# Optimization experiments

Measured on AMD Instinct MI355X. Metric: run time of the kernel, lower is better.

Reference implementation:

```python
import jax, jax.numpy as jnp
import numpy as np

B, T, D, F, H, HID, OUT = 256, 512, 768, 1024, 8, 512, 256
EPS = 1e-5

def setup_inputs() -> dict:
    key = jax.random.key(0)
    ks = jax.random.split(key, 16)
    s = lambda fan_in: 1.0 / np.sqrt(fan_in)
    return {
        "x": jax.random.normal(ks[0], (B, F), jnp.float32),
        "text_feat": jax.random.normal(ks[1], (B, T, D), jnp.float32),
        "attention_mask": jax.random.randint(ks[2], (B, T), 0, 2, jnp.int32),
        # cross-attention params (torch Linear weight layout [out,in])
        "Wq": jax.random.normal(ks[3], (F, F), jnp.float32) * s(F),
        "bq": jnp.zeros((F,), jnp.float32),
        "Wk": jax.random.normal(ks[4], (F, D), jnp.float32) * s(D),
        "bk": jnp.zeros((F,), jnp.float32),
        "Wv": jax.random.normal(ks[5], (F, D), jnp.float32) * s(D),
        "bv": jnp.zeros((F,), jnp.float32),
        "Wo": jax.random.normal(ks[6], (F, F), jnp.float32) * s(F),
        "bo": jnp.zeros((F,), jnp.float32),
        # MLP: hidden Linear -> BatchNorm1d -> GELU, then output Linear
        "W1": jax.random.normal(ks[7], (HID, F), jnp.float32) * s(F),
        "b1": jnp.zeros((HID,), jnp.float32),
        "gamma": jnp.ones((HID,), jnp.float32),
        "beta": jnp.zeros((HID,), jnp.float32),
        "W2": jax.random.normal(ks[8], (OUT, HID), jnp.float32) * s(HID),
        "b2": jnp.zeros((OUT,), jnp.float32),
    }

def _forward(x, text_feat, attention_mask, Wq, bq, Wk, bk, Wv, bv, Wo, bo,
             W1, b1, gamma, beta, W2, b2):
    d = F // H
    q = (x @ Wq.T + bq).reshape(B, H, d)                      # [B,H,d] (q_len=1)
    k = (text_feat @ Wk.T + bk).reshape(B, T, H, d)           # [B,T,H,d]
    v = (text_feat @ Wv.T + bv).reshape(B, T, H, d)
    attn = jnp.einsum('bhd,bthd->bht', q, k) / jnp.sqrt(jnp.float32(d))
    attn = jnp.where(attention_mask[:, None, :] == 0, -jnp.inf, attn)
    attn = jax.nn.softmax(attn, axis=-1)                       # [B,H,T]
    out = jnp.einsum('bht,bthd->bhd', attn, v).reshape(B, F)
    out = out @ Wo.T + bo
    # MLP hidden: linear -> BatchNorm1d (training batch stats) -> GELU (exact)
    h = out @ W1.T + b1
    mu = jnp.mean(h, axis=0)
    var = jnp.var(h, axis=0)
    h = (h - mu) / jnp.sqrt(var + EPS) * gamma + beta
    h = jax.nn.gelu(h, approximate=False)
    return h @ W2.T + b2

def reference(x, text_feat, attention_mask, Wq, bq, Wk, bk, Wv, bv, Wo, bo,
              W1, b1, gamma, beta, W2, b2):
    return _forward(x, text_feat, attention_mask, Wq, bq, Wk, bk, Wv, bv, Wo, bo,
                    W1, b1, gamma, beta, W2, b2)
```

## Files before the change

kernel.cpp:

```cpp
#include <hip/hip_runtime.h>
#include <math.h>

#define Bb   256
#define Tt   512
#define Dd   768
#define Ff   1024
#define Hh   8
#define HIDh 512
#define OUTo 256

__device__ __forceinline__ void tr_tile(const float* __restrict__ in,
                                        float* __restrict__ out,
                                        int R, int C, int cx, int ry,
                                        float (*tile)[33])
{
    int c0 = cx * 32, r0 = ry * 32;
    int tx = threadIdx.x & 31, ty = threadIdx.x >> 5;
#pragma unroll
    for (int i = 0; i < 32; i += 8)
        tile[ty + i][tx] = in[(size_t)(r0 + ty + i) * C + c0 + tx];
    __syncthreads();
#pragma unroll
    for (int i = 0; i < 32; i += 8)
        out[(size_t)(c0 + ty + i) * R + r0 + tx] = tile[tx][ty + i];
}

__global__ __launch_bounds__(256) void prep(const float* __restrict__ Wq, float* __restrict__ WqT,
                                            const float* __restrict__ Wo, float* __restrict__ WoT,
                                            const float* __restrict__ Wv, float* __restrict__ WvT,
                                            const float* __restrict__ W1, float* __restrict__ W1T,
                                            const float* __restrict__ W2, float* __restrict__ W2T,
                                            const float* __restrict__ Wk, float* __restrict__ WkT)
{
    __shared__ float tile[32][33];
    int idx = blockIdx.x;
    if (idx < 1024) {
        tr_tile(Wq, WqT, 1024, 1024, idx & 31, idx >> 5, tile);
    } else if (idx < 2048) {
        int i2 = idx - 1024;
        tr_tile(Wo, WoT, 1024, 1024, i2 & 31, i2 >> 5, tile);
    } else if (idx < 2816) {
        int i2 = idx - 2048;
        tr_tile(Wv, WvT, 1024, 768, i2 % 24, i2 / 24, tile);
    } else if (idx < 3328) {
        int i2 = idx - 2816;
        tr_tile(W1, W1T, 512, 1024, i2 & 31, i2 >> 5, tile);
    } else if (idx < 3456) {
        int i2 = idx - 3328;
        tr_tile(W2, W2T, 256, 512, i2 & 15, i2 >> 4, tile);
    } else {
        int i2 = idx - 3456;
        int i = i2 >> 3, h = i2 & 7;
        for (int j = threadIdx.x; j < 768; j += 256)
            WkT[(size_t)(i * 8 + h) * 768 + j] = Wk[(size_t)(h * 128 + i) * 768 + j];
    }
}

#define FMA16(acc, a, w0, w1, w2, w3)                         \
    acc.x = fmaf(a.x, w0.x, acc.x); acc.y = fmaf(a.x, w0.y, acc.y); \
    acc.z = fmaf(a.x, w0.z, acc.z); acc.w = fmaf(a.x, w0.w, acc.w); \
    acc.x = fmaf(a.y, w1.x, acc.x); acc.y = fmaf(a.y, w1.y, acc.y); \
    acc.z = fmaf(a.y, w1.z, acc.z); acc.w = fmaf(a.y, w1.w, acc.w); \
    acc.x = fmaf(a.z, w2.x, acc.x); acc.y = fmaf(a.z, w2.y, acc.y); \
    acc.z = fmaf(a.z, w2.z, acc.z); acc.w = fmaf(a.z, w2.w, acc.w); \
    acc.x = fmaf(a.w, w3.x, acc.x); acc.y = fmaf(a.w, w3.y, acc.y); \
    acc.z = fmaf(a.w, w3.z, acc.z); acc.w = fmaf(a.w, w3.w, acc.w);

template<int CT, int RT, int R, int KS>
__global__ __launch_bounds__(256, 4) void gemm_sk(const float* __restrict__ A, int strideA,
                                                  const float* __restrict__ Wt, int N,
                                                  float* __restrict__ Cslab, int M)
{
    constexpr int CG = CT / 4;
    constexpr int RG = RT / R;
    static_assert(CG * RG == 256, "bad tile");
    const int cg = threadIdx.x % CG;
    const int rg = threadIdx.x / CG;
    const int cb = blockIdx.x, rb = blockIdx.y, ks = blockIdx.z;
    const int n0 = cb * CT + cg * 4;
    const int r0 = rb * RT;
    const int k0 = ks * KS;

    __shared__ float As[RT][KS + 4];
    for (int e = threadIdx.x * 4; e < RT * KS; e += 1024) {
        int r = e / KS, k = e % KS;
        *(float4*)&As[r][k] = *(const float4*)&A[(size_t)(r0 + r) * strideA + k0 + k];
    }
    __syncthreads();

    float4 acc[R];
#pragma unroll
    for (int rr = 0; rr < R; ++rr) acc[rr] = make_float4(0.f, 0.f, 0.f, 0.f);
    const float* wp = Wt + (size_t)k0 * N + n0;
#pragma unroll 2
    for (int k = 0; k < KS; k += 4) {
        float4 w0 = *(const float4*)&wp[(size_t)(k + 0) * N];
        float4 w1 = *(const float4*)&wp[(size_t)(k + 1) * N];
        float4 w2 = *(const float4*)&wp[(size_t)(k + 2) * N];
        float4 w3 = *(const float4*)&wp[(size_t)(k + 3) * N];
#pragma unroll
        for (int rr = 0; rr < R; ++rr) {
            float4 a = *(const float4*)&As[rg * R + rr][k];
            FMA16(acc[rr], a, w0, w1, w2, w3)
        }
    }
    float* cp = Cslab + (size_t)ks * M * N;
#pragma unroll
    for (int rr = 0; rr < R; ++rr)
        *(float4*)&cp[(size_t)(r0 + rg * R + rr) * N + n0] = acc[rr];
}

template<int CT, int RT, int R, int KS, int S>
__global__ __launch_bounds__(256, 4) void gemm_skf(const float* __restrict__ slabs,
                                                   size_t slabstride, int strideA,
                                                   const float* __restrict__ bias,
                                                   const float* __restrict__ Wt, int N,
                                                   float* __restrict__ Cslab, int M)
{
    constexpr int CG = CT / 4;
    constexpr int RG = RT / R;
    static_assert(CG * RG == 256, "bad tile");
    const int cg = threadIdx.x % CG;
    const int rg = threadIdx.x / CG;
    const int cb = blockIdx.x, rb = blockIdx.y, ks = blockIdx.z;
    const int n0 = cb * CT + cg * 4;
    const int r0 = rb * RT;
    const int k0 = ks * KS;

    __shared__ float As[RT][KS + 4];
    for (int e = threadIdx.x * 4; e < RT * KS; e += 1024) {
        int r = e / KS, k = e % KS;
        float4 acc = *(const float4*)&bias[k0 + k];
#pragma unroll
        for (int s = 0; s < S; ++s) {
            float4 v = *(const float4*)&slabs[(size_t)s * slabstride + (size_t)(r0 + r) * strideA + k0 + k];
            acc.x += v.x; acc.y += v.y; acc.z += v.z; acc.w += v.w;
        }
        *(float4*)&As[r][k] = acc;
    }
    __syncthreads();

    float4 acc[R];
#pragma unroll
    for (int rr = 0; rr < R; ++rr) acc[rr] = make_float4(0.f, 0.f, 0.f, 0.f);
    const float* wp = Wt + (size_t)k0 * N + n0;
#pragma unroll 2
    for (int k = 0; k < KS; k += 4) {
        float4 w0 = *(const float4*)&wp[(size_t)(k + 0) * N];
        float4 w1 = *(const float4*)&wp[(size_t)(k + 1) * N];
        float4 w2 = *(const float4*)&wp[(size_t)(k + 2) * N];
        float4 w3 = *(const float4*)&wp[(size_t)(k + 3) * N];
#pragma unroll
        for (int rr = 0; rr < R; ++rr) {
            float4 a = *(const float4*)&As[rg * R + rr][k];
            FMA16(acc[rr], a, w0, w1, w2, w3)
        }
    }
    float* cp = Cslab + (size_t)ks * M * N;
#pragma unroll
    for (int rr = 0; rr < R; ++rr)
        *(float4*)&cp[(size_t)(r0 + rg * R + rr) * N + n0] = acc[rr];
}

__global__ __launch_bounds__(256, 4) void qk_gemm(const float* __restrict__ qslab,
                                                  const float* __restrict__ bq,
                                                  const float* __restrict__ WkT,
                                                  float* __restrict__ qkfull)
{
    const int cg = threadIdx.x & 15;
    const int rg = threadIdx.x >> 4;
    const int cb = blockIdx.x, rb = blockIdx.y;
    const int n0 = cb * 64 + cg * 4;
    const int r0 = rb * 16;
    const int aoff = ((cb * 64) / 768) * 128;

    __shared__ float As[16][132];
    for (int e = threadIdx.x * 4; e < 16 * 128; e += 1024) {
        int r = e >> 7, k = e & 127;
        float4 acc = *(const float4*)&bq[aoff + k];
#pragma unroll
        for (int s = 0; s < 8; ++s) {
            float4 v = *(const float4*)&qslab[(size_t)s * 262144 + (size_t)(r0 + r) * 1024 + aoff + k];
            acc.x += v.x; acc.y += v.y; acc.z += v.z; acc.w += v.w;
        }
        *(float4*)&As[r][k] = acc;
    }
    __syncthreads();

    float4 acc = make_float4(0.f, 0.f, 0.f, 0.f);
    const float* wp = WkT + n0;
#pragma unroll 4
    for (int k = 0; k < 128; k += 4) {
        float4 w0 = *(const float4*)&wp[(size_t)(k + 0) * 6144];
        float4 w1 = *(const float4*)&wp[(size_t)(k + 1) * 6144];
        float4 w2 = *(const float4*)&wp[(size_t)(k + 2) * 6144];
        float4 w3 = *(const float4*)&wp[(size_t)(k + 3) * 6144];
        float4 a = *(const float4*)&As[rg][k];
        FMA16(acc, a, w0, w1, w2, w3)
    }
    *(float4*)&qkfull[(size_t)(r0 + rg) * 6144 + n0] = acc;
}

__global__ __launch_bounds__(256, 2) void attn_part(const float* __restrict__ text,
                                                    const int* __restrict__ mask,
                                                    const float* __restrict__ qk,
                                                    float* __restrict__ pctx,
                                                    float* __restrict__ psum)
{
    const int bx   = blockIdx.x;
    const int b    = bx >> 2;
    const int qt   = bx & 3;
    const int tid  = threadIdx.x;
    const int wv   = tid >> 6;
    const int lane = tid & 63;

    __shared__ float qk_s[Hh][Dd];
    __shared__ float ctx_s[Hh][Dd];
    __shared__ float wsum_s[4][Hh];
    __shared__ int   list_s[128];
    __shared__ int   wcnt_s[2];

    const float* qkp = qk + (size_t)b * (Hh * Dd);
    float* qf = (float*)qk_s;
    float* cf = (float*)ctx_s;
    for (int e = tid * 4; e < Hh * Dd; e += 1024) {
        *(float4*)&qf[e] = *(const float4*)&qkp[e];
        *(float4*)&cf[e] = make_float4(0.f, 0.f, 0.f, 0.f);
    }

    int m = 0, pre = 0, t = 0;
    if (wv < 2) {
        t = qt * 128 + wv * 64 + lane;
        m = mask[(size_t)b * Tt + t];
        unsigned long long bal = __ballot(m != 0);
        pre = __popcll(bal & ((1ull << lane) - 1ull));
        if (lane == 0) wcnt_s[wv] = __popcll(bal);
    }
    __syncthreads();
    if (wv < 2 && m) {
        int base = wv ? wcnt_s[0] : 0;
        list_s[base + pre] = t;
    }
    __syncthreads();
    const int cnt = wcnt_s[0] + wcnt_s[1];

    float s[Hh] = {0.f, 0.f, 0.f, 0.f, 0.f, 0.f, 0.f, 0.f};
    float4 cr[Hh][3];
#pragma unroll
    for (int h = 0; h < Hh; ++h)
#pragma unroll
        for (int c = 0; c < 3; ++c) cr[h][c] = make_float4(0.f, 0.f, 0.f, 0.f);

    const float scale = 0.08838834764831845f;
    const float* tbase = text + (size_t)b * Tt * Dd;

    int e = wv;
    float4 xa0, xa1, xa2;
    if (e < cnt) {
        const float* tp = tbase + (size_t)list_s[e] * Dd + 4 * lane;
        xa0 = *(const float4*)(tp);
        xa1 = *(const float4*)(tp + 256);
        xa2 = *(const float4*)(tp + 512);
    }
    while (e < cnt) {
        int en = e + 4;
        float4 xb0 = xa0, xb1 = xa1, xb2 = xa2;
        if (en < cnt) {
            const float* tp = tbase + (size_t)list_s[en] * Dd + 4 * lane;
            xb0 = *(const float4*)(tp);
            xb1 = *(const float4*)(tp + 256);
            xb2 = *(const float4*)(tp + 512);
        }
        float p[Hh];
#pragma unroll
        for (int h = 0; h < Hh; ++h) {
            const float* qh = &qk_s[h][4 * lane];
            float4 a0 = *(const float4*)(qh);
            float4 a1 = *(const float4*)(qh + 256);
            float4 a2 = *(const float4*)(qh + 512);
            float acc;
            acc = a0.x * xa0.x;
            acc = fmaf(a0.y, xa0.y, acc);
            acc = fmaf(a0.z, xa0.z, acc);
            acc = fmaf(a0.w, xa0.w, acc);
            acc = fmaf(a1.x, xa1.x, acc);
            acc = fmaf(a1.y, xa1.y, acc);
            acc = fmaf(a1.z, xa1.z, acc);
            acc = fmaf(a1.w, xa1.w, acc);
            acc = fmaf(a2.x, xa2.x, acc);
            acc = fmaf(a2.y, xa2.y, acc);
            acc = fmaf(a2.z, xa2.z, acc);
            acc = fmaf(a2.w, xa2.w, acc);
            p[h] = acc;
        }
#pragma unroll
        for (int h = 0; h < Hh; ++h) {
            float v = p[h];
            v += __shfl_xor(v, 1);
            v += __shfl_xor(v, 2);
            v += __shfl_xor(v, 4);
            v += __shfl_xor(v, 8);
            v += __shfl_xor(v, 16);
            v += __shfl_xor(v, 32);
            float w = __expf(v * scale);
            s[h] += w;
            cr[h][0].x = fmaf(w, xa0.x, cr[h][0].x);
            cr[h][0].y = fmaf(w, xa0.y, cr[h][0].y);
            cr[h][0].z = fmaf(w, xa0.z, cr[h][0].z);
            cr[h][0].w = fmaf(w, xa0.w, cr[h][0].w);
            cr[h][1].x = fmaf(w, xa1.x, cr[h][1].x);
            cr[h][1].y = fmaf(w, xa1.y, cr[h][1].y);
            cr[h][1].z = fmaf(w, xa1.z, cr[h][1].z);
            cr[h][1].w = fmaf(w, xa1.w, cr[h][1].w);
            cr[h][2].x = fmaf(w, xa2.x, cr[h][2].x);
            cr[h][2].y = fmaf(w, xa2.y, cr[h][2].y);
            cr[h][2].z = fmaf(w, xa2.z, cr[h][2].z);
            cr[h][2].w = fmaf(w, xa2.w, cr[h][2].w);
        }
        xa0 = xb0; xa1 = xb1; xa2 = xb2;
        e = en;
    }

    if (lane == 0) {
#pragma unroll
        for (int h = 0; h < Hh; ++h) wsum_s[wv][h] = s[h];
    }

    for (int w4 = 0; w4 < 4; ++w4) {
        __syncthreads();
        if (wv == w4) {
#pragma unroll
            for (int h = 0; h < Hh; ++h) {
                float* cp = &ctx_s[h][4 * lane];
#pragma unroll
                for (int c = 0; c < 3; ++c) {
                    float4 cur = *(float4*)(cp + c * 256);
                    cur.x += cr[h][c].x;
                    cur.y += cr[h][c].y;
                    cur.z += cr[h][c].z;
                    cur.w += cr[h][c].w;
                    *(float4*)(cp + c * 256) = cur;
                }
            }
        }
    }
    __syncthreads();

    if (tid < Hh) {
        float S = wsum_s[0][tid] + wsum_s[1][tid] + wsum_s[2][tid] + wsum_s[3][tid];
        psum[(size_t)bx * Hh + tid] = S;
    }
    float* outp = pctx + (size_t)bx * (Hh * Dd);
    for (int e2 = tid * 4; e2 < Hh * Dd; e2 += 1024)
        *(float4*)&outp[e2] = *(const float4*)&cf[e2];
}

__global__ __launch_bounds__(256, 4) void v_gemm(const float* __restrict__ pctx,
                                                 const float* __restrict__ psum,
                                                 const float* __restrict__ WvT,
                                                 float* __restrict__ aoslab)
{
    const int cg = threadIdx.x & 31;
    const int rg = threadIdx.x >> 5;
    const int h = blockIdx.x, rb = blockIdx.y, ks = blockIdx.z;
    const int n0 = h * 128 + cg * 4;
    const int r0 = rb * 32;
    const int k0 = ks * 128;

    __shared__ float As[32][132];
    __shared__ float sv[32];

    if (threadIdx.x < 32) {
        int row = r0 + threadIdx.x;
        float S = 0.f;
#pragma unroll
        for (int i = 0; i < 4; ++i) S += psum[(size_t)(row * 4 + i) * Hh + h];
        sv[threadIdx.x] = 1.0f / S;
    }
    __syncthreads();
    for (int e = threadIdx.x * 4; e < 32 * 128; e += 1024) {
        int r = e >> 7, k = e & 127;
        size_t col = (size_t)h * 768 + k0 + k;
        float4 acc = make_float4(0.f, 0.f, 0.f, 0.f);
#pragma unroll
        for (int i = 0; i < 4; ++i) {
            float4 v = *(const float4*)&pctx[((size_t)(r0 + r) * 4 + i) * 6144 + col];
            acc.x += v.x; acc.y += v.y; acc.z += v.z; acc.w += v.w;
        }
        float svv = sv[r];
        acc.x *= svv; acc.y *= svv; acc.z *= svv; acc.w *= svv;
        *(float4*)&As[r][k] = acc;
    }
    __syncthreads();

    float4 acc[4];
#pragma unroll
    for (int rr = 0; rr < 4; ++rr) acc[rr] = make_float4(0.f, 0.f, 0.f, 0.f);
    const float* wp = WvT + (size_t)k0 * 1024 + n0;
#pragma unroll 2
    for (int k = 0; k < 128; k += 4) {
        float4 w0 = *(const float4*)&wp[(size_t)(k + 0) * 1024];
        float4 w1 = *(const float4*)&wp[(size_t)(k + 1) * 1024];
        float4 w2 = *(const float4*)&wp[(size_t)(k + 2) * 1024];
        float4 w3 = *(const float4*)&wp[(size_t)(k + 3) * 1024];
#pragma unroll
        for (int rr = 0; rr < 4; ++rr) {
            float4 a = *(const float4*)&As[rg * 4 + rr][k];
            FMA16(acc[rr], a, w0, w1, w2, w3)
        }
    }
    float* cp = aoslab + (size_t)ks * 262144;
#pragma unroll
    for (int rr = 0; rr < 4; ++rr)
        *(float4*)&cp[(size_t)(r0 + rg * 4 + rr) * 1024 + n0] = acc[rr];
}

__global__ __launch_bounds__(256) void bn_stats2(const float* __restrict__ h1slab,
                                                 const float* __restrict__ b1,
                                                 const float* __restrict__ gamma,
                                                 const float* __restrict__ beta,
                                                 float* __restrict__ scl,
                                                 float* __restrict__ shf)
{
    int c8 = threadIdx.x & 7, rg = threadIdx.x >> 3;
    int c = blockIdx.x * 8 + c8;
    float bias = b1[c];
    float sum = 0.f, sq = 0.f;
    for (int r = rg; r < Bb; r += 32) {
        float v = bias;
#pragma unroll
        for (int s = 0; s < 8; ++s)
            v += h1slab[(size_t)s * 131072 + (size_t)r * HIDh + c];
        sum += v;
        sq = fmaf(v, v, sq);
    }
    __shared__ float ss[32][8], sq_[32][8];
    ss[rg][c8] = sum; sq_[rg][c8] = sq;
    for (int off = 16; off > 0; off >>= 1) {
        __syncthreads();
        if (rg < off) { ss[rg][c8] += ss[rg + off][c8]; sq_[rg][c8] += sq_[rg + off][c8]; }
    }
    __syncthreads();
    if (rg == 0) {
        float mu  = ss[0][c8] * (1.0f / Bb);
        float var = sq_[0][c8] * (1.0f / Bb) - mu * mu;
        float g   = gamma[c] * rsqrtf(var + 1e-5f);
        scl[c] = g;
        shf[c] = fmaf(-mu, g, beta[c]);
    }
}

__global__ __launch_bounds__(256, 4) void gelu2(const float* __restrict__ h1slab,
                                                const float* __restrict__ b1,
                                                const float* __restrict__ scl,
                                                const float* __restrict__ shf,
                                                const float* __restrict__ W2T,
                                                const float* __restrict__ b2,
                                                float* __restrict__ out)
{
    const int cg = threadIdx.x & 15;
    const int rg = threadIdx.x >> 4;
    const int n0 = blockIdx.x * 64 + cg * 4;
    const int r0 = blockIdx.y * 16;

    __shared__ float As[16][132];
    float4 acc = make_float4(0.f, 0.f, 0.f, 0.f);

    for (int k0 = 0; k0 < HIDh; k0 += 128) {
        __syncthreads();
        for (int e = threadIdx.x * 4; e < 2048; e += 1024) {
            int r = e >> 7, k = e & 127;
            float4 v = *(const float4*)&b1[k0 + k];
#pragma unroll
            for (int s = 0; s < 8; ++s) {
                float4 u = *(const float4*)&h1slab[(size_t)s * 131072 + (size_t)(r0 + r) * HIDh + k0 + k];
                v.x += u.x; v.y += u.y; v.z += u.z; v.w += u.w;
            }
            float4 sc = *(const float4*)&scl[k0 + k];
            float4 sh = *(const float4*)&shf[k0 + k];
            float4 z;
            z.x = fmaf(v.x, sc.x, sh.x);
            z.y = fmaf(v.y, sc.y, sh.y);
            z.z = fmaf(v.z, sc.z, sh.z);
            z.w = fmaf(v.w, sc.w, sh.w);
            z.x = 0.5f * z.x * (1.0f + erff(z.x * 0.70710678118654752f));
            z.y = 0.5f * z.y * (1.0f + erff(z.y * 0.70710678118654752f));
            z.z = 0.5f * z.z * (1.0f + erff(z.z * 0.70710678118654752f));
            z.w = 0.5f * z.w * (1.0f + erff(z.w * 0.70710678118654752f));
            *(float4*)&As[r][k] = z;
        }
        __syncthreads();
        const float* wp = W2T + (size_t)k0 * OUTo + n0;
#pragma unroll 2
        for (int k = 0; k < 128; k += 4) {
            float4 w0 = *(const float4*)&wp[(size_t)(k + 0) * OUTo];
            float4 w1 = *(const float4*)&wp[(size_t)(k + 1) * OUTo];
            float4 w2 = *(const float4*)&wp[(size_t)(k + 2) * OUTo];
            float4 w3 = *(const float4*)&wp[(size_t)(k + 3) * OUTo];
            float4 a = *(const float4*)&As[rg][k];
            FMA16(acc, a, w0, w1, w2, w3)
        }
    }

    float4 bvv = *(const float4*)&b2[n0];
    acc.x += bvv.x; acc.y += bvv.y; acc.z += bvv.z; acc.w += bvv.w;
    *(float4*)&out[(size_t)(r0 + rg) * OUTo + n0] = acc;
}

extern "C" void kernel_launch(void* const* d_in, const int* in_sizes, int n_in,
                              void* d_out, int out_size, void* d_ws, size_t ws_size,
                              hipStream_t stream)
{
    const float* x     = (const float*)d_in[0];
    const float* text  = (const float*)d_in[1];
    const int*   amask = (const int*)d_in[2];
    const float* Wq    = (const float*)d_in[3];
    const float* bq    = (const float*)d_in[4];
    const float* Wk    = (const float*)d_in[5];
    const float* Wv    = (const float*)d_in[7];
    const float* bv    = (const float*)d_in[8];
    const float* Wo    = (const float*)d_in[9];
    const float* bo    = (const float*)d_in[10];
    const float* W1    = (const float*)d_in[11];
    const float* b1    = (const float*)d_in[12];
    const float* gamma = (const float*)d_in[13];
    const float* beta  = (const float*)d_in[14];
    const float* W2    = (const float*)d_in[15];
    const float* b2    = (const float*)d_in[16];

    float* ws     = (float*)d_ws;
    float* WqT    = ws;
    float* WoT    = WqT    + 1048576;
    float* WkT    = WoT    + 1048576;
    float* WvT    = WkT    + 786432;
    float* W1T    = WvT    + 786432;
    float* W2T    = W1T    + 524288;
    float* qslab  = W2T    + 131072;
    float* qkfull = qslab  + 2097152;
    float* pctx   = qkfull + 1572864;
    float* psum   = pctx   + 6291456;
    float* aoslab = psum   + 8192;
    float* oslab  = aoslab + 1572864;
    float* h1slab = oslab  + 2097152;
    float* scl    = h1slab + 1048576;
    float* shf    = scl    + 512;

    prep<<<4480, 256, 0, stream>>>(Wq, WqT, Wo, WoT, Wv, WvT, W1, W1T, W2, W2T, Wk, WkT);

    gemm_sk<128, 32, 4, 128><<<dim3(8, 8, 8), 256, 0, stream>>>(x, 1024, WqT, 1024, qslab, 256);

    qk_gemm<<<dim3(96, 16), 256, 0, stream>>>(qslab, bq, WkT, qkfull);

    attn_part<<<1024, 256, 0, stream>>>(text, amask, qkfull, pctx, psum);

    v_gemm<<<dim3(8, 8, 6), 256, 0, stream>>>(pctx, psum, WvT, aoslab);

    gemm_skf<128, 32, 4, 128, 6><<<dim3(8, 8, 8), 256, 0, stream>>>(aoslab, 262144, 1024, bv, WoT, 1024, oslab, 256);

    gemm_skf<64, 32, 2, 128, 8><<<dim3(8, 8, 8), 256, 0, stream>>>(oslab, 262144, 1024, bo, W1T, 512, h1slab, 256);

    bn_stats2<<<64, 256, 0, stream>>>(h1slab, b1, gamma, beta, scl, shf);

    gelu2<<<dim3(4, 16), 256, 0, stream>>>(h1slab, b1, scl, shf, W2T, b2, (float*)d_out);
}
```

Before: 251.9 us.

## Split split-K reductions into separate kernels, rework attention and GEMM tiles

Split-K partial sums are now reduced by dedicated reduce_add kernels instead of being summed redundantly inside every consumer block. GEMM tiles shrink and grids grow for more parallelism, and unroll factors go up. The attention kernel now uses 512-thread blocks over half the sequence and processes two tokens per iteration. Weight transposes and the Wk copy use float4 accesses. The cost is extra kernel launches and extra workspace round trips through global memory.

```diff
diff --git a/kernel.cpp b/kernel.cpp
--- a/kernel.cpp
+++ b/kernel.cpp
@@ -9,20 +9,26 @@
 #define HIDh 512
 #define OUTo 256
 
-__device__ __forceinline__ void tr_tile(const float* __restrict__ in,
-                                        float* __restrict__ out,
-                                        int R, int C, int cx, int ry,
-                                        float (*tile)[33])
+__device__ __forceinline__ void tr_tile4(const float* __restrict__ in,
+                                         float* __restrict__ out,
+                                         int R, int C, int cx, int ry,
+                                         float (*tile)[33])
 {
     int c0 = cx * 32, r0 = ry * 32;
-    int tx = threadIdx.x & 31, ty = threadIdx.x >> 5;
-#pragma unroll
-    for (int i = 0; i < 32; i += 8)
-        tile[ty + i][tx] = in[(size_t)(r0 + ty + i) * C + c0 + tx];
-    __syncthreads();
-#pragma unroll
-    for (int i = 0; i < 32; i += 8)
-        out[(size_t)(c0 + ty + i) * R + r0 + tx] = tile[tx][ty + i];
+    int r  = threadIdx.x >> 3;
+    int c4 = (threadIdx.x & 7) * 4;
+    float4 v = *(const float4*)&in[(size_t)(r0 + r) * C + c0 + c4];
+    tile[r][c4 + 0] = v.x;
+    tile[r][c4 + 1] = v.y;
+    tile[r][c4 + 2] = v.z;
+    tile[r][c4 + 3] = v.w;
+    __syncthreads();
+    float4 o;
+    o.x = tile[c4 + 0][r];
+    o.y = tile[c4 + 1][r];
+    o.z = tile[c4 + 2][r];
+    o.w = tile[c4 + 3][r];
+    *(float4*)&out[(size_t)(c0 + r) * R + r0 + c4] = o;
 }
 
 __global__ __launch_bounds__(256) void prep(const float* __restrict__ Wq, float* __restrict__ WqT,
@@ -35,24 +41,27 @@
     __shared__ float tile[32][33];
     int idx = blockIdx.x;
     if (idx < 1024) {
-        tr_tile(Wq, WqT, 1024, 1024, idx & 31, idx >> 5, tile);
+        tr_tile4(Wq, WqT, 1024, 1024, idx & 31, idx >> 5, tile);
     } else if (idx < 2048) {
         int i2 = idx - 1024;
-        tr_tile(Wo, WoT, 1024, 1024, i2 & 31, i2 >> 5, tile);
+        tr_tile4(Wo, WoT, 1024, 1024, i2 & 31, i2 >> 5, tile);
     } else if (idx < 2816) {
         int i2 = idx - 2048;
-        tr_tile(Wv, WvT, 1024, 768, i2 % 24, i2 / 24, tile);
+        tr_tile4(Wv, WvT, 1024, 768, i2 % 24, i2 / 24, tile);
     } else if (idx < 3328) {
         int i2 = idx - 2816;
-        tr_tile(W1, W1T, 512, 1024, i2 & 31, i2 >> 5, tile);
+        tr_tile4(W1, W1T, 512, 1024, i2 & 31, i2 >> 5, tile);
     } else if (idx < 3456) {
         int i2 = idx - 3328;
-        tr_tile(W2, W2T, 256, 512, i2 & 15, i2 >> 4, tile);
+        tr_tile4(W2, W2T, 256, 512, i2 & 15, i2 >> 4, tile);
     } else {
         int i2 = idx - 3456;
         int i = i2 >> 3, h = i2 & 7;
-        for (int j = threadIdx.x; j < 768; j += 256)
-            WkT[(size_t)(i * 8 + h) * 768 + j] = Wk[(size_t)(h * 128 + i) * 768 + j];
+        if (threadIdx.x < 192) {
+            int j = threadIdx.x * 4;
+            *(float4*)&WkT[(size_t)(i * 8 + h) * 768 + j] =
+                *(const float4*)&Wk[(size_t)(h * 128 + i) * 768 + j];
+        }
     }
 }
 
@@ -76,10 +85,9 @@
     static_assert(CG * RG == 256, "bad tile");
     const int cg = threadIdx.x % CG;
     const int rg = threadIdx.x / CG;
-    const int cb = blockIdx.x, rb = blockIdx.y, ks = blockIdx.z;
-    const int n0 = cb * CT + cg * 4;
-    const int r0 = rb * RT;
-    const int k0 = ks * KS;
+    const int n0 = blockIdx.x * CT + cg * 4;
+    const int r0 = blockIdx.y * RT;
+    const int k0 = blockIdx.z * KS;
 
     __shared__ float As[RT][KS + 4];
     for (int e = threadIdx.x * 4; e < RT * KS; e += 1024) {
@@ -92,7 +100,7 @@
 #pragma unroll
     for (int rr = 0; rr < R; ++rr) acc[rr] = make_float4(0.f, 0.f, 0.f, 0.f);
     const float* wp = Wt + (size_t)k0 * N + n0;
-#pragma unroll 2
+#pragma unroll 4
     for (int k = 0; k < KS; k += 4) {
         float4 w0 = *(const float4*)&wp[(size_t)(k + 0) * N];
         float4 w1 = *(const float4*)&wp[(size_t)(k + 1) * N];
@@ -104,66 +112,30 @@
             FMA16(acc[rr], a, w0, w1, w2, w3)
         }
     }
-    float* cp = Cslab + (size_t)ks * M * N;
+    float* cp = Cslab + (size_t)blockIdx.z * M * N;
 #pragma unroll
     for (int rr = 0; rr < R; ++rr)
         *(float4*)&cp[(size_t)(r0 + rg * R + rr) * N + n0] = acc[rr];
 }
 
-template<int CT, int RT, int R, int KS, int S>
-__global__ __launch_bounds__(256, 4) void gemm_skf(const float* __restrict__ slabs,
-                                                   size_t slabstride, int strideA,
-                                                   const float* __restrict__ bias,
-                                                   const float* __restrict__ Wt, int N,
-                                                   float* __restrict__ Cslab, int M)
-{
-    constexpr int CG = CT / 4;
-    constexpr int RG = RT / R;
-    static_assert(CG * RG == 256, "bad tile");
-    const int cg = threadIdx.x % CG;
-    const int rg = threadIdx.x / CG;
-    const int cb = blockIdx.x, rb = blockIdx.y, ks = blockIdx.z;
-    const int n0 = cb * CT + cg * 4;
-    const int r0 = rb * RT;
-    const int k0 = ks * KS;
-
-    __shared__ float As[RT][KS + 4];
-    for (int e = threadIdx.x * 4; e < RT * KS; e += 1024) {
-        int r = e / KS, k = e % KS;
-        float4 acc = *(const float4*)&bias[k0 + k];
-#pragma unroll
-        for (int s = 0; s < S; ++s) {
-            float4 v = *(const float4*)&slabs[(size_t)s * slabstride + (size_t)(r0 + r) * strideA + k0 + k];
-            acc.x += v.x; acc.y += v.y; acc.z += v.z; acc.w += v.w;
-        }
-        *(float4*)&As[r][k] = acc;
-    }
-    __syncthreads();
-
-    float4 acc[R];
-#pragma unroll
-    for (int rr = 0; rr < R; ++rr) acc[rr] = make_float4(0.f, 0.f, 0.f, 0.f);
-    const float* wp = Wt + (size_t)k0 * N + n0;
-#pragma unroll 2
-    for (int k = 0; k < KS; k += 4) {
-        float4 w0 = *(const float4*)&wp[(size_t)(k + 0) * N];
-        float4 w1 = *(const float4*)&wp[(size_t)(k + 1) * N];
-        float4 w2 = *(const float4*)&wp[(size_t)(k + 2) * N];
-        float4 w3 = *(const float4*)&wp[(size_t)(k + 3) * N];
-#pragma unroll
-        for (int rr = 0; rr < R; ++rr) {
-            float4 a = *(const float4*)&As[rg * R + rr][k];
-            FMA16(acc[rr], a, w0, w1, w2, w3)
-        }
-    }
-    float* cp = Cslab + (size_t)ks * M * N;
-#pragma unroll
-    for (int rr = 0; rr < R; ++rr)
-        *(float4*)&cp[(size_t)(r0 + rg * R + rr) * N + n0] = acc[rr];
-}
-
-__global__ __launch_bounds__(256, 4) void qk_gemm(const float* __restrict__ qslab,
-                                                  const float* __restrict__ bq,
+template<int S>
+__global__ __launch_bounds__(256) void reduce_add(const float* __restrict__ slabs,
+                                                  size_t slabstride,
+                                                  const float* __restrict__ bias,
+                                                  float* __restrict__ out, int N, int total)
+{
+    int i4 = (blockIdx.x * 256 + threadIdx.x) * 4;
+    if (i4 >= total) return;
+    float4 acc = *(const float4*)&bias[i4 % N];
+#pragma unroll
+    for (int s = 0; s < S; ++s) {
+        float4 v = *(const float4*)(slabs + (size_t)s * slabstride + i4);
+        acc.x += v.x; acc.y += v.y; acc.z += v.z; acc.w += v.w;
+    }
+    *(float4*)&out[i4] = acc;
+}
+
+__global__ __launch_bounds__(256, 4) void qk_gemm(const float* __restrict__ qfull,
                                                   const float* __restrict__ WkT,
                                                   float* __restrict__ qkfull)
 {
@@ -175,15 +147,9 @@
     const int aoff = ((cb * 64) / 768) * 128;
 
     __shared__ float As[16][132];
-    for (int e = threadIdx.x * 4; e < 16 * 128; e += 1024) {
+    for (int e = threadIdx.x * 4; e < 2048; e += 1024) {
         int r = e >> 7, k = e & 127;
-        float4 acc = *(const float4*)&bq[aoff + k];
-#pragma unroll
-        for (int s = 0; s < 8; ++s) {
-            float4 v = *(const float4*)&qslab[(size_t)s * 262144 + (size_t)(r0 + r) * 1024 + aoff + k];
-            acc.x += v.x; acc.y += v.y; acc.z += v.z; acc.w += v.w;
-        }
-        *(float4*)&As[r][k] = acc;
+        *(float4*)&As[r][k] = *(const float4*)&qfull[(size_t)(r0 + r) * 1024 + aoff + k];
     }
     __syncthreads();
 
@@ -201,48 +167,68 @@
     *(float4*)&qkfull[(size_t)(r0 + rg) * 6144 + n0] = acc;
 }
 
-__global__ __launch_bounds__(256, 2) void attn_part(const float* __restrict__ text,
+__device__ __forceinline__ float dot12(float4 a0, float4 a1, float4 a2,
+                                       float4 x0, float4 x1, float4 x2)
+{
+    float acc;
+    acc = a0.x * x0.x;
+    acc = fmaf(a0.y, x0.y, acc);
+    acc = fmaf(a0.z, x0.z, acc);
+    acc = fmaf(a0.w, x0.w, acc);
+    acc = fmaf(a1.x, x1.x, acc);
+    acc = fmaf(a1.y, x1.y, acc);
+    acc = fmaf(a1.z, x1.z, acc);
+    acc = fmaf(a1.w, x1.w, acc);
+    acc = fmaf(a2.x, x2.x, acc);
+    acc = fmaf(a2.y, x2.y, acc);
+    acc = fmaf(a2.z, x2.z, acc);
+    acc = fmaf(a2.w, x2.w, acc);
+    return acc;
+}
+
+__global__ __launch_bounds__(512, 1) void attn_part(const float* __restrict__ text,
                                                     const int* __restrict__ mask,
                                                     const float* __restrict__ qk,
                                                     float* __restrict__ pctx,
                                                     float* __restrict__ psum)
 {
     const int bx   = blockIdx.x;
-    const int b    = bx >> 2;
-    const int qt   = bx & 3;
+    const int b    = bx >> 1;
+    const int hf   = bx & 1;
     const int tid  = threadIdx.x;
     const int wv   = tid >> 6;
     const int lane = tid & 63;
 
     __shared__ float qk_s[Hh][Dd];
     __shared__ float ctx_s[Hh][Dd];
-    __shared__ float wsum_s[4][Hh];
-    __shared__ int   list_s[128];
-    __shared__ int   wcnt_s[2];
+    __shared__ float wsum_s[8][Hh];
+    __shared__ int   list_s[256];
+    __shared__ int   wcnt_s[4];
 
     const float* qkp = qk + (size_t)b * (Hh * Dd);
     float* qf = (float*)qk_s;
     float* cf = (float*)ctx_s;
-    for (int e = tid * 4; e < Hh * Dd; e += 1024) {
+    for (int e = tid * 4; e < Hh * Dd; e += 2048) {
         *(float4*)&qf[e] = *(const float4*)&qkp[e];
         *(float4*)&cf[e] = make_float4(0.f, 0.f, 0.f, 0.f);
     }
 
     int m = 0, pre = 0, t = 0;
-    if (wv < 2) {
-        t = qt * 128 + wv * 64 + lane;
+    if (wv < 4) {
+        t = hf * 256 + wv * 64 + lane;
         m = mask[(size_t)b * Tt + t];
         unsigned long long bal = __ballot(m != 0);
         pre = __popcll(bal & ((1ull << lane) - 1ull));
         if (lane == 0) wcnt_s[wv] = __popcll(bal);
     }
     __syncthreads();
-    if (wv < 2 && m) {
-        int base = wv ? wcnt_s[0] : 0;
+    if (wv < 4 && m) {
+        int base = 0;
+        for (int w = 0; w < wv; ++w) base += wcnt_s[w];
         list_s[base + pre] = t;
     }
     __syncthreads();
-    const int cnt = wcnt_s[0] + wcnt_s[1];
+    const int cnt = wcnt_s[0] + wcnt_s[1] + wcnt_s[2] + wcnt_s[3];
 
     float s[Hh] = {0.f, 0.f, 0.f, 0.f, 0.f, 0.f, 0.f, 0.f};
     float4 cr[Hh][3];
@@ -254,70 +240,96 @@
     const float scale = 0.08838834764831845f;
     const float* tbase = text + (size_t)b * Tt * Dd;
 
-    int e = wv;
-    float4 xa0, xa1, xa2;
+    int e = wv * 2;
+    bool vy = false;
+    float4 xa0, xa1, xa2, ya0, ya1, ya2;
     if (e < cnt) {
         const float* tp = tbase + (size_t)list_s[e] * Dd + 4 * lane;
         xa0 = *(const float4*)(tp);
         xa1 = *(const float4*)(tp + 256);
         xa2 = *(const float4*)(tp + 512);
+        vy = (e + 1 < cnt);
+        const float* tq = tbase + (size_t)list_s[vy ? e + 1 : e] * Dd + 4 * lane;
+        ya0 = *(const float4*)(tq);
+        ya1 = *(const float4*)(tq + 256);
+        ya2 = *(const float4*)(tq + 512);
     }
     while (e < cnt) {
-        int en = e + 4;
-        float4 xb0 = xa0, xb1 = xa1, xb2 = xa2;
-        if (en < cnt) {
+        int en = e + 16;
+        bool nv  = en < cnt;
+        bool nvy = (en + 1 < cnt);
+        float4 xb0 = xa0, xb1 = xa1, xb2 = xa2, yb0 = ya0, yb1 = ya1, yb2 = ya2;
+        if (nv) {
             const float* tp = tbase + (size_t)list_s[en] * Dd + 4 * lane;
             xb0 = *(const float4*)(tp);
             xb1 = *(const float4*)(tp + 256);
             xb2 = *(const float4*)(tp + 512);
-        }
-        float p[Hh];
+            const float* tq = tbase + (size_t)list_s[nvy ? en + 1 : en] * Dd + 4 * lane;
+            yb0 = *(const float4*)(tq);
+            yb1 = *(const float4*)(tq + 256);
+            yb2 = *(const float4*)(tq + 512);
+        }
+
+        float px[Hh], py[Hh];
 #pragma unroll
         for (int h = 0; h < Hh; ++h) {
             const float* qh = &qk_s[h][4 * lane];
             float4 a0 = *(const float4*)(qh);
             float4 a1 = *(const float4*)(qh + 256);
             float4 a2 = *(const float4*)(qh + 512);
-            float acc;
-            acc = a0.x * xa0.x;
-            acc = fmaf(a0.y, xa0.y, acc);
-            acc = fmaf(a0.z, xa0.z, acc);
-            acc = fmaf(a0.w, xa0.w, acc);
-            acc = fmaf(a1.x, xa1.x, acc);
-            acc = fmaf(a1.y, xa1.y, acc);
-            acc = fmaf(a1.z, xa1.z, acc);
-            acc = fmaf(a1.w, xa1.w, acc);
-            acc = fmaf(a2.x, xa2.x, acc);
-            acc = fmaf(a2.y, xa2.y, acc);
-            acc = fmaf(a2.z, xa2.z, acc);
-            acc = fmaf(a2.w, xa2.w, acc);
-            p[h] = acc;
+            px[h] = dot12(a0, a1, a2, xa0, xa1, xa2);
+            py[h] = dot12(a0, a1, a2, ya0, ya1, ya2);
         }
 #pragma unroll
         for (int h = 0; h < Hh; ++h) {
-            float v = p[h];
+            float v = px[h];
             v += __shfl_xor(v, 1);
             v += __shfl_xor(v, 2);
             v += __shfl_xor(v, 4);
             v += __shfl_xor(v, 8);
             v += __shfl_xor(v, 16);
             v += __shfl_xor(v, 32);
-            float w = __expf(v * scale);
-            s[h] += w;
-            cr[h][0].x = fmaf(w, xa0.x, cr[h][0].x);
-            cr[h][0].y = fmaf(w, xa0.y, cr[h][0].y);
-            cr[h][0].z = fmaf(w, xa0.z, cr[h][0].z);
-            cr[h][0].w = fmaf(w, xa0.w, cr[h][0].w);
-            cr[h][1].x = fmaf(w, xa1.x, cr[h][1].x);
-            cr[h][1].y = fmaf(w, xa1.y, cr[h][1].y);
-            cr[h][1].z = fmaf(w, xa1.z, cr[h][1].z);
-            cr[h][1].w = fmaf(w, xa1.w, cr[h][1].w);
-            cr[h][2].x = fmaf(w, xa2.x, cr[h][2].x);
-            cr[h][2].y = fmaf(w, xa2.y, cr[h][2].y);
-            cr[h][2].z = fmaf(w, xa2.z, cr[h][2].z);
-            cr[h][2].w = fmaf(w, xa2.w, cr[h][2].w);
+            float u = py[h];
+            u += __shfl_xor(u, 1);
+            u += __shfl_xor(u, 2);
+            u += __shfl_xor(u, 4);
+            u += __shfl_xor(u, 8);
+            u += __shfl_xor(u, 16);
+            u += __shfl_xor(u, 32);
+            float wx = __expf(v * scale);
+            s[h] += wx;
+            cr[h][0].x = fmaf(wx, xa0.x, cr[h][0].x);
+            cr[h][0].y = fmaf(wx, xa0.y, cr[h][0].y);
+            cr[h][0].z = fmaf(wx, xa0.z, cr[h][0].z);
+            cr[h][0].w = fmaf(wx, xa0.w, cr[h][0].w);
+            cr[h][1].x = fmaf(wx, xa1.x, cr[h][1].x);
+            cr[h][1].y = fmaf(wx, xa1.y, cr[h][1].y);
+            cr[h][1].z = fmaf(wx, xa1.z, cr[h][1].z);
+            cr[h][1].w = fmaf(wx, xa1.w, cr[h][1].w);
+            cr[h][2].x = fmaf(wx, xa2.x, cr[h][2].x);
+            cr[h][2].y = fmaf(wx, xa2.y, cr[h][2].y);
+            cr[h][2].z = fmaf(wx, xa2.z, cr[h][2].z);
+            cr[h][2].w = fmaf(wx, xa2.w, cr[h][2].w);
+            if (vy) {
+                float wy = __expf(u * scale);
+                s[h] += wy;
+                cr[h][0].x = fmaf(wy, ya0.x, cr[h][0].x);
+                cr[h][0].y = fmaf(wy, ya0.y, cr[h][0].y);
+                cr[h][0].z = fmaf(wy, ya0.z, cr[h][0].z);
+                cr[h][0].w = fmaf(wy, ya0.w, cr[h][0].w);
+                cr[h][1].x = fmaf(wy, ya1.x, cr[h][1].x);
+                cr[h][1].y = fmaf(wy, ya1.y, cr[h][1].y);
+                cr[h][1].z = fmaf(wy, ya1.z, cr[h][1].z);
+                cr[h][1].w = fmaf(wy, ya1.w, cr[h][1].w);
+                cr[h][2].x = fmaf(wy, ya2.x, cr[h][2].x);
+                cr[h][2].y = fmaf(wy, ya2.y, cr[h][2].y);
+                cr[h][2].z = fmaf(wy, ya2.z, cr[h][2].z);
+                cr[h][2].w = fmaf(wy, ya2.w, cr[h][2].w);
+            }
         }
         xa0 = xb0; xa1 = xb1; xa2 = xb2;
+        ya0 = yb0; ya1 = yb1; ya2 = yb2;
+        vy = nvy;
         e = en;
     }
 
@@ -326,32 +338,30 @@
         for (int h = 0; h < Hh; ++h) wsum_s[wv][h] = s[h];
     }
 
-    for (int w4 = 0; w4 < 4; ++w4) {
+    for (int r = 0; r < 8; ++r) {
         __syncthreads();
-        if (wv == w4) {
-#pragma unroll
-            for (int h = 0; h < Hh; ++h) {
-                float* cp = &ctx_s[h][4 * lane];
-#pragma unroll
-                for (int c = 0; c < 3; ++c) {
-                    float4 cur = *(float4*)(cp + c * 256);
-                    cur.x += cr[h][c].x;
-                    cur.y += cr[h][c].y;
-                    cur.z += cr[h][c].z;
-                    cur.w += cr[h][c].w;
-                    *(float4*)(cp + c * 256) = cur;
-                }
-            }
+        int h = (wv + r) & 7;
+        float* cp = &ctx_s[h][4 * lane];
+#pragma unroll
+        for (int c = 0; c < 3; ++c) {
+            float4 cur = *(float4*)(cp + c * 256);
+            cur.x += cr[h][c].x;
+            cur.y += cr[h][c].y;
+            cur.z += cr[h][c].z;
+            cur.w += cr[h][c].w;
+            *(float4*)(cp + c * 256) = cur;
         }
     }
     __syncthreads();
 
     if (tid < Hh) {
-        float S = wsum_s[0][tid] + wsum_s[1][tid] + wsum_s[2][tid] + wsum_s[3][tid];
+        float S = 0.f;
+#pragma unroll
+        for (int w = 0; w < 8; ++w) S += wsum_s[w][tid];
         psum[(size_t)bx * Hh + tid] = S;
     }
     float* outp = pctx + (size_t)bx * (Hh * Dd);
-    for (int e2 = tid * 4; e2 < Hh * Dd; e2 += 1024)
+    for (int e2 = tid * 4; e2 < Hh * Dd; e2 += 2048)
         *(float4*)&outp[e2] = *(const float4*)&cf[e2];
 }
 
@@ -364,59 +374,56 @@
     const int rg = threadIdx.x >> 5;
     const int h = blockIdx.x, rb = blockIdx.y, ks = blockIdx.z;
     const int n0 = h * 128 + cg * 4;
-    const int r0 = rb * 32;
+    const int r0 = rb * 16;
     const int k0 = ks * 128;
 
-    __shared__ float As[32][132];
-    __shared__ float sv[32];
-
-    if (threadIdx.x < 32) {
+    __shared__ float As[16][132];
+    __shared__ float sv[16];
+
+    if (threadIdx.x < 16) {
         int row = r0 + threadIdx.x;
-        float S = 0.f;
-#pragma unroll
-        for (int i = 0; i < 4; ++i) S += psum[(size_t)(row * 4 + i) * Hh + h];
+        float S = psum[(size_t)(row * 2) * Hh + h] + psum[(size_t)(row * 2 + 1) * Hh + h];
         sv[threadIdx.x] = 1.0f / S;
     }
     __syncthreads();
-    for (int e = threadIdx.x * 4; e < 32 * 128; e += 1024) {
+    for (int e = threadIdx.x * 4; e < 2048; e += 1024) {
         int r = e >> 7, k = e & 127;
         size_t col = (size_t)h * 768 + k0 + k;
-        float4 acc = make_float4(0.f, 0.f, 0.f, 0.f);
-#pragma unroll
-        for (int i = 0; i < 4; ++i) {
-            float4 v = *(const float4*)&pctx[((size_t)(r0 + r) * 4 + i) * 6144 + col];
-            acc.x += v.x; acc.y += v.y; acc.z += v.z; acc.w += v.w;
-        }
+        float4 a = *(const float4*)&pctx[(size_t)(r0 + r) * 2 * 6144 + col];
+        float4 c = *(const float4*)&pctx[((size_t)(r0 + r) * 2 + 1) * 6144 + col];
         float svv = sv[r];
-        acc.x *= svv; acc.y *= svv; acc.z *= svv; acc.w *= svv;
-        *(float4*)&As[r][k] = acc;
-    }
-    __syncthreads();
-
-    float4 acc[4];
-#pragma unroll
-    for (int rr = 0; rr < 4; ++rr) acc[rr] = make_float4(0.f, 0.f, 0.f, 0.f);
+        float4 o;
+        o.x = (a.x + c.x) * svv;
+        o.y = (a.y + c.y) * svv;
+        o.z = (a.z + c.z) * svv;
+        o.w = (a.w + c.w) * svv;
+        *(float4*)&As[r][k] = o;
+    }
+    __syncthreads();
+
+    float4 acc[2];
+    acc[0] = make_float4(0.f, 0.f, 0.f, 0.f);
+    acc[1] = make_float4(0.f, 0.f, 0.f, 0.f);
     const float* wp = WvT + (size_t)k0 * 1024 + n0;
-#pragma unroll 2
+#pragma unroll 4
     for (int k = 0; k < 128; k += 4) {
         float4 w0 = *(const float4*)&wp[(size_t)(k + 0) * 1024];
         float4 w1 = *(const float4*)&wp[(size_t)(k + 1) * 1024];
         float4 w2 = *(const float4*)&wp[(size_t)(k + 2) * 1024];
         float4 w3 = *(const float4*)&wp[(size_t)(k + 3) * 1024];
 #pragma unroll
-        for (int rr = 0; rr < 4; ++rr) {
-            float4 a = *(const float4*)&As[rg * 4 + rr][k];
+        for (int rr = 0; rr < 2; ++rr) {
+            float4 a = *(const float4*)&As[rg * 2 + rr][k];
             FMA16(acc[rr], a, w0, w1, w2, w3)
         }
     }
     float* cp = aoslab + (size_t)ks * 262144;
 #pragma unroll
-    for (int rr = 0; rr < 4; ++rr)
-        *(float4*)&cp[(size_t)(r0 + rg * 4 + rr) * 1024 + n0] = acc[rr];
-}
-
-__global__ __launch_bounds__(256) void bn_stats2(const float* __restrict__ h1slab,
-                                                 const float* __restrict__ b1,
+    for (int rr = 0; rr < 2; ++rr)
+        *(float4*)&cp[(size_t)(r0 + rg * 2 + rr) * 1024 + n0] = acc[rr];
+}
+
+__global__ __launch_bounds__(256) void bn_stats2(const float* __restrict__ h1full,
                                                  const float* __restrict__ gamma,
                                                  const float* __restrict__ beta,
                                                  float* __restrict__ scl,
@@ -424,13 +431,9 @@
 {
     int c8 = threadIdx.x & 7, rg = threadIdx.x >> 3;
     int c = blockIdx.x * 8 + c8;
-    float bias = b1[c];
     float sum = 0.f, sq = 0.f;
     for (int r = rg; r < Bb; r += 32) {
-        float v = bias;
-#pragma unroll
-        for (int s = 0; s < 8; ++s)
-            v += h1slab[(size_t)s * 131072 + (size_t)r * HIDh + c];
+        float v = h1full[(size_t)r * HIDh + c];
         sum += v;
         sq = fmaf(v, v, sq);
     }
@@ -450,8 +453,7 @@
     }
 }
 
-__global__ __launch_bounds__(256, 4) void gelu2(const float* __restrict__ h1slab,
-                                                const float* __restrict__ b1,
+__global__ __launch_bounds__(256, 4) void gelu2(const float* __restrict__ h1full,
                                                 const float* __restrict__ scl,
                                                 const float* __restrict__ shf,
                                                 const float* __restrict__ W2T,
@@ -470,12 +472,7 @@
         __syncthreads();
         for (int e = threadIdx.x * 4; e < 2048; e += 1024) {
             int r = e >> 7, k = e & 127;
-            float4 v = *(const float4*)&b1[k0 + k];
-#pragma unroll
-            for (int s = 0; s < 8; ++s) {
-                float4 u = *(const float4*)&h1slab[(size_t)s * 131072 + (size_t)(r0 + r) * HIDh + k0 + k];
-                v.x += u.x; v.y += u.y; v.z += u.z; v.w += u.w;
-            }
+            float4 v  = *(const float4*)&h1full[(size_t)(r0 + r) * HIDh + k0 + k];
             float4 sc = *(const float4*)&scl[k0 + k];
             float4 sh = *(const float4*)&shf[k0 + k];
             float4 z;
@@ -491,7 +488,7 @@
         }
         __syncthreads();
         const float* wp = W2T + (size_t)k0 * OUTo + n0;
-#pragma unroll 2
+#pragma unroll 4
         for (int k = 0; k < 128; k += 4) {
             float4 w0 = *(const float4*)&wp[(size_t)(k + 0) * OUTo];
             float4 w1 = *(const float4*)&wp[(size_t)(k + 1) * OUTo];
@@ -536,30 +533,38 @@
     float* W1T    = WvT    + 786432;
     float* W2T    = W1T    + 524288;
     float* qslab  = W2T    + 131072;
-    float* qkfull = qslab  + 2097152;
+    float* qfull  = qslab  + 2097152;
+    float* qkfull = qfull  + 262144;
     float* pctx   = qkfull + 1572864;
-    float* psum   = pctx   + 6291456;
-    float* aoslab = psum   + 8192;
-    float* oslab  = aoslab + 1572864;
-    float* h1slab = oslab  + 2097152;
-    float* scl    = h1slab + 1048576;
+    float* psum   = pctx   + 3145728;
+    float* aoslab = psum   + 4096;
+    float* aofull = aoslab + 1572864;
+    float* oslab  = aofull + 262144;
+    float* ofull  = oslab  + 2097152;
+    float* h1slab = ofull  + 262144;
+    float* h1full = h1slab + 1048576;
+    float* scl    = h1full + 131072;
     float* shf    = scl    + 512;
 
     prep<<<4480, 256, 0, stream>>>(Wq, WqT, Wo, WoT, Wv, WvT, W1, W1T, W2, W2T, Wk, WkT);
 
-    gemm_sk<128, 32, 4, 128><<<dim3(8, 8, 8), 256, 0, stream>>>(x, 1024, WqT, 1024, qslab, 256);
-
-    qk_gemm<<<dim3(96, 16), 256, 0, stream>>>(qslab, bq, WkT, qkfull);
-
-    attn_part<<<1024, 256, 0, stream>>>(text, amask, qkfull, pctx, psum);
-
-    v_gemm<<<dim3(8, 8, 6), 256, 0, stream>>>(pctx, psum, WvT, aoslab);
-
-    gemm_skf<128, 32, 4, 128, 6><<<dim3(8, 8, 8), 256, 0, stream>>>(aoslab, 262144, 1024, bv, WoT, 1024, oslab, 256);
-
-    gemm_skf<64, 32, 2, 128, 8><<<dim3(8, 8, 8), 256, 0, stream>>>(oslab, 262144, 1024, bo, W1T, 512, h1slab, 256);
-
-    bn_stats2<<<64, 256, 0, stream>>>(h1slab, b1, gamma, beta, scl, shf);
-
-    gelu2<<<dim3(4, 16), 256, 0, stream>>>(h1slab, b1, scl, shf, W2T, b2, (float*)d_out);
-}
+    gemm_sk<64, 32, 2, 128><<<dim3(16, 8, 8), 256, 0, stream>>>(x, 1024, WqT, 1024, qslab, 256);
+    reduce_add<8><<<256, 256, 0, stream>>>(qslab, 262144, bq, qfull, 1024, 262144);
+
+    qk_gemm<<<dim3(96, 16), 256, 0, stream>>>(qfull, WkT, qkfull);
+
+    attn_part<<<512, 512, 0, stream>>>(text, amask, qkfull, pctx, psum);
+
+    v_gemm<<<dim3(8, 16, 6), 256, 0, stream>>>(pctx, psum, WvT, aoslab);
+    reduce_add<6><<<256, 256, 0, stream>>>(aoslab, 262144, bv, aofull, 1024, 262144);
+
+    gemm_sk<64, 32, 2, 128><<<dim3(16, 8, 8), 256, 0, stream>>>(aofull, 1024, WoT, 1024, oslab, 256);
+    reduce_add<8><<<256, 256, 0, stream>>>(oslab, 262144, bo, ofull, 1024, 262144);
+
+    gemm_sk<64, 16, 1, 128><<<dim3(8, 16, 8), 256, 0, stream>>>(ofull, 1024, W1T, 512, h1slab, 256);
+    reduce_add<8><<<128, 256, 0, stream>>>(h1slab, 131072, b1, h1full, 512, 131072);
+
+    bn_stats2<<<64, 256, 0, stream>>>(h1full, gamma, beta, scl, shf);
+
+    gelu2<<<dim3(4, 16), 256, 0, stream>>>(h1full, scl, shf, W2T, b2, (float*)d_out);
+}
```

Result: slower. 339.1 us (+34.6%).
